# Kernel optimization log

Measured on AMD Instinct MI355X. Metric: run time of the kernel, lower is better.

## Reference

```python
import jax, jax.numpy as jnp
import numpy as np

K = 3          # spline order
NUM = 32       # grid intervals G
IN_DIM = 256
OUT_DIM = 512
BATCH = 2048


def _b_spline_basis(x, grid, k):
    """Cox-de-Boor recursion. x: (B, I); grid: (I, G+2k+1) -> (B, I, G+k)."""
    xg = x[:, :, None]                      # (B, I, 1)
    g = grid[None, :, :]                    # (1, I, G+2k+1)
    val = ((xg >= g[:, :, :-1]) & (xg < g[:, :, 1:])).astype(x.dtype)
    for p in range(1, k + 1):
        left = (xg - g[:, :, :-(p + 1)]) / (g[:, :, p:-1] - g[:, :, :-(p + 1)])
        right = (g[:, :, p + 1:] - xg) / (g[:, :, p + 1:] - g[:, :, 1:-p])
        val = left * val[:, :, :-1] + right * val[:, :, 1:]
    return val                               # (B, I, G+k)


def setup_inputs() -> dict:
    key = jax.random.key(0)
    k1, k2, k3 = jax.random.split(key, 3)
    x = jax.random.normal(k1, (BATCH, IN_DIM), dtype=jnp.float32)
    # uniform grid on [-1, 1], extended by k knots on each side (extend_grid)
    base = np.linspace(-1.0, 1.0, NUM + 1)
    h = 2.0 / NUM
    ext = np.concatenate([base[0] - h * np.arange(K, 0, -1), base,
                          base[-1] + h * np.arange(1, K + 1)]).astype(np.float32)
    grid = jnp.tile(jnp.asarray(ext)[None, :], (IN_DIM, 1))  # (I, G+2k+1)
    coef = 0.1 * jax.random.normal(k2, (IN_DIM, OUT_DIM, NUM + K), dtype=jnp.float32)
    scale_base = jax.random.normal(k3, (IN_DIM, OUT_DIM), dtype=jnp.float32) / np.sqrt(IN_DIM).astype(np.float32)
    scale_sp = jnp.ones((IN_DIM, OUT_DIM), dtype=jnp.float32) / np.sqrt(IN_DIM).astype(np.float32)
    mask = jnp.ones((IN_DIM, OUT_DIM), dtype=jnp.float32)
    return {"x": x, "grid": grid, "coef": coef,
            "scale_base": scale_base, "scale_sp": scale_sp, "mask": mask}


def reference(x, grid, coef, scale_base, scale_sp, mask):
    base = jax.nn.silu(x)                                   # b(x) residual, (B, I)
    bases = _b_spline_basis(x, grid, K)                     # (B, I, G+k)
    # coef2curve: einsum('ijk,jlk->ijl') in pykan -> (B, I, O)
    y = jnp.einsum('bik,iok->bio', bases, coef)
    y = scale_base[None, :, :] * base[:, :, None] + scale_sp[None, :, :] * y
    y = mask[None, :, :] * y
    return jnp.sum(y, axis=1)                               # (B, O)
```

## Files before the change

kernel.cpp:

```cpp
#include <hip/hip_runtime.h>
#include <math.h>

#define BATCH   2048
#define IN_DIM  256
#define OUT_DIM 512
#define NK      35
#define KS      48
#define KG      6
#define BTILE   128
#define OTILE   128
#define ICHUNK  32
#define NSPLIT  8
#define COEFS_BYTES ((size_t)IN_DIM * OUT_DIM * KS * 2)
#define PART_ELEMS  ((size_t)BATCH * OUT_DIM)

__device__ __forceinline__ unsigned short f2bf(float x) {
    unsigned u = __float_as_uint(x);
    u += 0x7FFF + ((u >> 16) & 1);
    return (unsigned short)(u >> 16);
}
__device__ __forceinline__ float bf2f(unsigned short h) {
    return __uint_as_float(((unsigned)h) << 16);
}
__device__ __forceinline__ unsigned pack2(unsigned short a, unsigned short b) {
    return (unsigned)a | ((unsigned)b << 16);
}

typedef __bf16 bf16x8 __attribute__((ext_vector_type(8)));
typedef float  f32x16 __attribute__((ext_vector_type(16)));
typedef unsigned int u32;

__device__ __forceinline__ void gload_lds16(const void* g, void* l) {
    __builtin_amdgcn_global_load_lds((const __attribute__((address_space(1))) u32*)g,
                                     (__attribute__((address_space(3))) u32*)l, 16, 0, 0);
}

#define PR 32
__global__ __launch_bounds__(256) void kan_prep(
    const float* __restrict__ coef,
    const float* __restrict__ scale_base,
    const float* __restrict__ scale_sp,
    const float* __restrict__ mask,
    unsigned short* __restrict__ coefS)
{
    __shared__ float sc[PR * NK];
    __shared__ float sspm[PR], ssbm[PR];
    const int t    = threadIdx.x;
    const int row0 = blockIdx.x * PR;

    {
        const float4* csrc = (const float4*)(coef + (size_t)row0 * NK);
        float4* cdst = (float4*)sc;
        cdst[t] = csrc[t];
        if (t < 24) cdst[t + 256] = csrc[t + 256];
    }
    if (t < PR) {
        float m = mask[row0 + t];
        sspm[t] = scale_sp[row0 + t] * m;
        ssbm[t] = scale_base[row0 + t] * m;
    }
    __syncthreads();

    if (t < PR * 6) {
        int r = t / 6;
        int q = t - r * 6;
        float spm = sspm[r];
        const float* c = sc + r * NK;
        uint4 v = make_uint4(0u, 0u, 0u, 0u);
        if (q < 4) {
            const float* cq = c + q * 8;
            v.x = pack2(f2bf(cq[0] * spm), f2bf(cq[1] * spm));
            v.y = pack2(f2bf(cq[2] * spm), f2bf(cq[3] * spm));
            v.z = pack2(f2bf(cq[4] * spm), f2bf(cq[5] * spm));
            v.w = pack2(f2bf(cq[6] * spm), f2bf(cq[7] * spm));
        } else if (q == 4) {
            float sbm = ssbm[r];
            unsigned short hi = f2bf(sbm);
            unsigned short lo = f2bf(sbm - bf2f(hi));
            v.x = pack2(f2bf(c[32] * spm), f2bf(c[33] * spm));
            v.y = pack2(f2bf(c[34] * spm), 0);
            v.z = pack2(hi, hi);
            v.w = pack2(lo, 0);
        }
        int g = row0 + r;
        size_t di = ((size_t)(((g >> 9) * 4 + ((g >> 7) & 3)) * 6 + q)) * 128
                  + (size_t)(g & 127);
        ((uint4*)coefS)[di] = v;
    }
}

__global__ __launch_bounds__(256, 2) void kan_mfma(
    const float* __restrict__ x,
    const unsigned short* __restrict__ coefS,
    float* __restrict__ part)
{
    __shared__ __align__(16) short sA[2 * BTILE * KS];
    __shared__ __align__(16) short sB[2 * OTILE * KS];

    const int t    = threadIdx.x;
    const int w    = t >> 6;
    const int lane = t & 63;
    const int l31  = lane & 31, lh = lane >> 5;
    const int wr   = w & 1;
    const int wc   = w >> 1;
    const int o0   = blockIdx.x * OTILE;
    const int b0   = blockIdx.y * BTILE;
    const int ic0  = blockIdx.z * ICHUNK;
    const bool bTh = (t >= 128);
    const int wbase = t & 64;

    {
        uint4 z = make_uint4(0, 0, 0, 0);
        #pragma unroll
        for (int u = 0; u < 6; ++u) {
            int idx = t + 256 * u;
            if (idx < (2 * BTILE * KS * 2) / 16) ((uint4*)sA)[idx] = z;
        }
    }

    f32x16 acc00 = {}, acc01 = {}, acc10 = {}, acc11 = {};

    float xreg = 0.0f;
    int ojb0 = 0, ojb1 = 0;

    auto stageA = [&](short* abuf, int row, float xv, int& ojbn) {
        #pragma unroll
        for (int qq = 0; qq < 4; ++qq) {
            int k = ojbn + qq;
            abuf[((k >> 3) * BTILE + row) * 8 + (k & 7)] = 0;
        }
        float xn = (xv + 1.1875f) * 16.0f;
        float jf = floorf(xn);
        int   j  = (int)jf;
        float u  = xn - jf;
        bool valid = (xn >= 0.0f) && (j <= 37);
        float u2 = u * u, u3 = u2 * u;
        float w0 = (1.0f / 6.0f) * (1.0f - 3.0f * u + 3.0f * u2 - u3);
        float w1 = (1.0f / 6.0f) * (3.0f * u3 - 6.0f * u2 + 4.0f);
        float w2 = (1.0f / 6.0f) * (-3.0f * u3 + 3.0f * u2 + 3.0f * u + 1.0f);
        float w3 = (1.0f / 6.0f) * u3;
        int jb = j - 3;
        if (valid) {
            if ((unsigned)jb < 35u) {
                int k = jb;     abuf[((k >> 3) * BTILE + row) * 8 + (k & 7)] = f2bf(w0);
            }
            if ((unsigned)(jb + 1) < 35u) {
                int k = jb + 1; abuf[((k >> 3) * BTILE + row) * 8 + (k & 7)] = f2bf(w1);
            }
            if ((unsigned)(jb + 2) < 35u) {
                int k = jb + 2; abuf[((k >> 3) * BTILE + row) * 8 + (k & 7)] = f2bf(w2);
            }
            if ((unsigned)(jb + 3) < 35u) {
                int k = jb + 3; abuf[((k >> 3) * BTILE + row) * 8 + (k & 7)] = f2bf(w3);
            }
        }
        ojbn = min(max(jb, 0), 31);
        float sig = 1.0f / (1.0f + __expf(-xv));
        float s   = xv * sig;
        unsigned short shi = f2bf(s);
        unsigned short slo = f2bf(s - bf2f(shi));
        short* k4 = abuf + (4 * BTILE + row) * 8;
        *(unsigned int*)(k4 + 4) = pack2(shi, slo);
        k4[6] = shi;
    };

    auto issueB = [&](int i, int buf) {
        const char* gsrc = (const char*)coefS
                         + ((size_t)i * 4 + (o0 >> 7)) * (KG * OTILE * 8 * 2);
        #pragma unroll
        for (int q = 0; q < 6; ++q) {
            int slot = wbase + (t & 63) + 128 * q;
            gload_lds16(gsrc + slot * 16,
                        (void*)(sB + buf * (OTILE * KS) + (wbase + 128 * q) * 8));
        }
    };

    __syncthreads();

    if (!bTh) {
        float x0 = x[(size_t)(b0 + t) * IN_DIM + ic0];
        stageA(sA, t, x0, ojb0);
        xreg = x[(size_t)(b0 + t) * IN_DIM + ic0 + 1];
    } else {
        issueB(ic0, 0);
    }
    __syncthreads();

    auto body = [&](int it, int cur, int nxt, int& ojbn) {
        if (bTh && it + 1 < ICHUNK) issueB(ic0 + it + 1, nxt);

        const short* Ab = sA + cur * (BTILE * KS) + (lh * BTILE + wr * 64 + l31) * 8;
        const short* Bb = sB + cur * (OTILE * KS) + (lh * OTILE + wc * 64 + l31) * 8;
        #pragma unroll
        for (int s = 0; s < 3; ++s) {
            bf16x8 a0 = *(const bf16x8*)(Ab + s * (2 * BTILE * 8));
            bf16x8 a1 = *(const bf16x8*)(Ab + s * (2 * BTILE * 8) + 32 * 8);
            bf16x8 b0 = *(const bf16x8*)(Bb + s * (2 * OTILE * 8));
            bf16x8 b1 = *(const bf16x8*)(Bb + s * (2 * OTILE * 8) + 32 * 8);
            acc00 = __builtin_amdgcn_mfma_f32_32x32x16_bf16(a0, b0, acc00, 0, 0, 0);
            acc01 = __builtin_amdgcn_mfma_f32_32x32x16_bf16(a0, b1, acc01, 0, 0, 0);
            acc10 = __builtin_amdgcn_mfma_f32_32x32x16_bf16(a1, b0, acc10, 0, 0, 0);
            acc11 = __builtin_amdgcn_mfma_f32_32x32x16_bf16(a1, b1, acc11, 0, 0, 0);
        }

        if (!bTh && it + 1 < ICHUNK) {
            stageA(sA + nxt * (BTILE * KS), t, xreg, ojbn);
            if (it + 2 < ICHUNK)
                xreg = x[(size_t)(b0 + t) * IN_DIM + ic0 + it + 2];
        }
        __syncthreads();
    };

    for (int itp = 0; itp < ICHUNK / 2; ++itp) {
        body(2 * itp,     0, 1, ojb1);
        body(2 * itp + 1, 1, 0, ojb0);
    }

    float* tp = (float*)sA + w * (32 * 36);
    float* pdst = part + (size_t)blockIdx.z * PART_ELEMS;
    #pragma unroll
    for (int r = 0; r < 2; ++r) {
        #pragma unroll
        for (int c = 0; c < 2; ++c) {
            const f32x16& acc = (r == 0) ? ((c == 0) ? acc00 : acc01)
                                         : ((c == 0) ? acc10 : acc11);
            #pragma unroll
            for (int reg = 0; reg < 16; ++reg) {
                int row = (reg & 3) + 8 * (reg >> 2) + 4 * lh;
                tp[row * 36 + l31] = acc[reg];
            }
            int cc = (lane & 7) * 4;
            #pragma unroll
            for (int j = 0; j < 4; ++j) {
                int rr = j * 8 + (lane >> 3);
                float4 v = *(float4*)&tp[rr * 36 + cc];
                int rowg = b0 + wr * 64 + r * 32 + rr;
                int colg = o0 + wc * 64 + c * 32 + cc;
                *(float4*)&pdst[(size_t)rowg * OUT_DIM + colg] = v;
            }
        }
    }
}

__global__ __launch_bounds__(256) void kan_reduce(
    const float4* __restrict__ part, float4* __restrict__ out)
{
    const size_t e = (size_t)blockIdx.x * 256 + threadIdx.x;
    float4 s = part[e];
    #pragma unroll
    for (int z = 1; z < NSPLIT; ++z) {
        float4 v = part[(size_t)z * (PART_ELEMS / 4) + e];
        s.x += v.x; s.y += v.y; s.z += v.z; s.w += v.w;
    }
    out[e] = s;
}

extern "C" void kernel_launch(void* const* d_in, const int* in_sizes, int n_in,
                              void* d_out, int out_size, void* d_ws, size_t ws_size,
                              hipStream_t stream) {
    const float* x          = (const float*)d_in[0];
    const float* coef       = (const float*)d_in[2];
    const float* scale_base = (const float*)d_in[3];
    const float* scale_sp   = (const float*)d_in[4];
    const float* mask       = (const float*)d_in[5];
    unsigned short* coefS   = (unsigned short*)d_ws;
    float* part             = (float*)((char*)d_ws + COEFS_BYTES);

    kan_prep<<<dim3(IN_DIM * OUT_DIM / PR), dim3(256), 0, stream>>>(
        coef, scale_base, scale_sp, mask, coefS);
    kan_mfma<<<dim3(OUT_DIM / OTILE, BATCH / BTILE, NSPLIT), dim3(256), 0, stream>>>(
        x, coefS, part);
    kan_reduce<<<dim3(BATCH * OUT_DIM / 4 / 256), dim3(256), 0, stream>>>(
        (const float4*)part, (float4*)d_out);
}
```

Baseline: 120.1 us.

## Deepen coefficient prefetch to four LDS buffers with partial vmcnt waits

Moves the B-tile (coefficient) staging from double buffering to a 4-deep ring, issuing loads three iterations ahead. The full __syncthreads is replaced by explicit s_waitcnt vmcnt(12)/lgkmcnt(0) plus s_barrier, so loader waves only wait for the oldest outstanding tile. This is meant to hide global-to-LDS latency behind the MFMA work. In exchange, LDS use grows, which may reduce occupancy under launch_bounds(256,2), and correctness now depends on the hand-counted vmcnt value.

```diff
diff --git a/kernel.cpp b/kernel.cpp
--- a/kernel.cpp
+++ b/kernel.cpp
@@ -11,6 +11,7 @@
 #define OTILE   128
 #define ICHUNK  32
 #define NSPLIT  8
+#define NBUF    4
 #define COEFS_BYTES ((size_t)IN_DIM * OUT_DIM * KS * 2)
 #define PART_ELEMS  ((size_t)BATCH * OUT_DIM)
 
@@ -95,7 +96,7 @@
     float* __restrict__ part)
 {
     __shared__ __align__(16) short sA[2 * BTILE * KS];
-    __shared__ __align__(16) short sB[2 * OTILE * KS];
+    __shared__ __align__(16) short sB[NBUF * OTILE * KS];
 
     const int t    = threadIdx.x;
     const int w    = t >> 6;
@@ -182,15 +183,25 @@
         stageA(sA, t, x0, ojb0);
         xreg = x[(size_t)(b0 + t) * IN_DIM + ic0 + 1];
     } else {
-        issueB(ic0, 0);
-    }
-    __syncthreads();
-
-    auto body = [&](int it, int cur, int nxt, int& ojbn) {
-        if (bTh && it + 1 < ICHUNK) issueB(ic0 + it + 1, nxt);
-
+        issueB(ic0,     0);
+        issueB(ic0 + 1, 1);
+        issueB(ic0 + 2, 2);
+    }
+    if (bTh) asm volatile("s_waitcnt vmcnt(12)" ::: "memory");
+    else     asm volatile("s_waitcnt lgkmcnt(0)" ::: "memory");
+    __builtin_amdgcn_s_barrier();
+    __builtin_amdgcn_sched_barrier(0);
+
+    auto body = [&](int it, int& ojbn) {
+        if (bTh && it + 1 < ICHUNK) {
+            int ip3 = (it + 3 < ICHUNK) ? (it + 3) : (ICHUNK - 1);
+            issueB(ic0 + ip3, (it + 3) & (NBUF - 1));
+        }
+
+        const int cur = it & 1;
         const short* Ab = sA + cur * (BTILE * KS) + (lh * BTILE + wr * 64 + l31) * 8;
-        const short* Bb = sB + cur * (OTILE * KS) + (lh * OTILE + wc * 64 + l31) * 8;
+        const short* Bb = sB + (it & (NBUF - 1)) * (OTILE * KS)
+                        + (lh * OTILE + wc * 64 + l31) * 8;
         #pragma unroll
         for (int s = 0; s < 3; ++s) {
             bf16x8 a0 = *(const bf16x8*)(Ab + s * (2 * BTILE * 8));
@@ -204,17 +215,25 @@
         }
 
         if (!bTh && it + 1 < ICHUNK) {
-            stageA(sA + nxt * (BTILE * KS), t, xreg, ojbn);
+            stageA(sA + (cur ^ 1) * (BTILE * KS), t, xreg, ojbn);
             if (it + 2 < ICHUNK)
                 xreg = x[(size_t)(b0 + t) * IN_DIM + ic0 + it + 2];
         }
-        __syncthreads();
+
+        if (it + 1 < ICHUNK) {
+            if (bTh) asm volatile("s_waitcnt vmcnt(12)" ::: "memory");
+            else     asm volatile("s_waitcnt lgkmcnt(0)" ::: "memory");
+            __builtin_amdgcn_s_barrier();
+            __builtin_amdgcn_sched_barrier(0);
+        }
     };
 
     for (int itp = 0; itp < ICHUNK / 2; ++itp) {
-        body(2 * itp,     0, 1, ojb1);
-        body(2 * itp + 1, 1, 0, ojb0);
-    }
+        body(2 * itp,     ojb1);
+        body(2 * itp + 1, ojb0);
+    }
+
+    __syncthreads();
 
     float* tp = (float*)sA + w * (32 * 36);
     float* pdst = part + (size_t)blockIdx.z * PART_ELEMS;
```

Measured after the change: 119.5 us. Within noise of the previous version (-0.6%).
